# Kernel optimization log

Measured on AMD Instinct MI355X. Metric: run time of the kernel, lower is better.

Reference implementation:

```python
import jax, jax.numpy as jnp
import numpy as np

LAT_T, LAT_H, LAT_W = 16, 44, 80  # hard-coded latent grid in preprocess_mask


def _preprocess_mask(mask):
    """mask: [T, H, W, B] float video mask -> [B, S] binary mask, S = 16*44*80.
    Mirrors torch trilinear interpolate (align_corners=False) per temporal chunk."""
    m = jnp.transpose(mask, (3, 0, 1, 2))[:, None]  # [B,1,T,H,W]
    B, _, T, _, _ = m.shape
    tgt = (B, 1, 1, LAT_H, LAT_W)
    pieces = [jax.image.resize(m[:, :, :1], tgt, 'trilinear', antialias=False)]
    for wi in range(1, T, 8):
        pieces.append(jax.image.resize(m[:, :, wi:wi + 8], tgt, 'trilinear', antialias=False))
    mm = jnp.concatenate(pieces, axis=2)[:, 0]  # [B,16,44,80]
    return (mm > 0.5).astype(jnp.float32).reshape(B, -1)  # [B,S]


def setup_inputs() -> dict:
    key = jax.random.key(0)
    ks = jax.random.split(key, 6)
    B, S, H, D, P, R = 1, 56320, 8, 64, 128, 2
    T, MH, MW = 121, 88, 160
    return {
        'q': jax.random.normal(ks[0], (B, S, H, D), jnp.float32),
        'k': jax.random.normal(ks[1], (B, P, H, D), jnp.float32),
        'v': jax.random.normal(ks[2], (B, P, H, D), jnp.float32),
        'regional_k': jax.random.normal(ks[3], (R, B, P, H, D), jnp.float32),
        'regional_v': jax.random.normal(ks[4], (R, B, P, H, D), jnp.float32),
        'region_masks': jax.random.uniform(ks[5], (R, T, MH, MW, B), jnp.float32),
    }


def reference(q, k, v, regional_k, regional_v, region_masks):
    B, S, H, D = q.shape
    P = k.shape[1]
    R = regional_k.shape[0]
    scale = D ** -0.5
    base_ratio = 0.5

    # per-region binary masks over the latent sequence: [R,B,S]
    masks = jnp.stack([_preprocess_mask(region_masks[i]) for i in range(R)], axis=0)
    masks_b = masks > 0.5
    global_mask = masks.sum(axis=0) == 0  # [B,S] queries covered by no region
    # allowed[b,s,r]: segment r of combined KV (r=0 global prompt, r>=1 region r-1)
    allowed = jnp.concatenate([global_mask[..., None], jnp.moveaxis(masks_b, 0, -1)], axis=-1)  # [B,S,R+1]

    combined_k = jnp.concatenate([k[None], regional_k], axis=0)  # [R+1,B,P,H,D]
    combined_v = jnp.concatenate([v[None], regional_v], axis=0)

    # regional pass: scores [B,H,S,R+1,P], additive -inf bias per segment
    scores = jnp.einsum('bshd,rbphd->bhsrp', q, combined_k) * scale
    scores = jnp.where(allowed[:, None, :, :, None], scores, -jnp.inf)
    p = jax.nn.softmax(scores.reshape(B, H, S, (R + 1) * P), axis=-1)
    out_reg = jnp.einsum('bhsrp,rbphd->bshd', p.reshape(B, H, S, R + 1, P), combined_v)

    # base pass: plain cross attention over the global prompt
    s_base = jnp.einsum('bshd,bphd->bhsp', q, k) * scale
    out_base = jnp.einsum('bhsp,bphd->bshd', jax.nn.softmax(s_base, axis=-1), v)

    out = out_reg * (1.0 - base_ratio) + out_base * base_ratio
    return out.reshape(B, S, H * D)
```

## Files before the change

### kernel.cpp

```cpp
#include <hip/hip_runtime.h>

typedef short short8  __attribute__((ext_vector_type(8)));
typedef float f32x4   __attribute__((ext_vector_type(4)));
typedef float f32x16  __attribute__((ext_vector_type(16)));

#define MFMA32(A,B,C) __builtin_amdgcn_mfma_f32_32x32x16_bf16((A),(B),(C),0,0,0)

__device__ __forceinline__ short bf16bits(float f){
  return (short)__builtin_bit_cast(unsigned short, static_cast<__bf16>(f));
}

#define EXP_SCORE(s, BIAS) __builtin_amdgcn_exp2f(__builtin_fmaf((s), 0.18033688011112042f, (BIAS)))
#define EXP_C2 (-11.541560327111707f)

__global__ __launch_bounds__(256) void prep_kernel(const float* __restrict__ rm,
                                                   const float* __restrict__ k,
                                                   const float* __restrict__ v,
                                                   const float* __restrict__ rk,
                                                   const float* __restrict__ rv,
                                                   unsigned* __restrict__ allowed,
                                                   unsigned short* __restrict__ Kb,
                                                   unsigned short* __restrict__ VT){
  const int bid = blockIdx.x;
  if (bid < 220){
    int s = bid*256 + threadIdx.x;
    if (s >= 56320) return;
    int t = s / 3520;
    int rem = s - t*3520;
    int i = rem / 80;
    int j = rem - i*80;
    int y = 2*i, x = 2*j;
    bool bin[2];
    #pragma unroll
    for (int r=0;r<2;r++){
      const float* base = rm + (size_t)r*121*88*160;
      float acc;
      if (t == 0){
        const float* p0 = base + (size_t)(0*88 + y)*160 + x;
        acc = 0.25f*(p0[0]+p0[1]+p0[160]+p0[161]);
      } else {
        const float* pa = base + (size_t)((8*t-4)*88 + y)*160 + x;
        const float* pb = base + (size_t)((8*t-3)*88 + y)*160 + x;
        acc = 0.125f*(pa[0]+pa[1]+pa[160]+pa[161] + pb[0]+pb[1]+pb[160]+pb[161]);
      }
      bin[r] = acc > 0.5f;
    }
    unsigned bits = (bin[0]||bin[1]) ? 0u : 1u;
    if (bin[0]) bits |= 2u;
    if (bin[1]) bits |= 4u;
    allowed[s] = bits;
  } else {
    int idx = (bid-220)*256 + threadIdx.x;
    if (idx >= 3*128*8*64) return;
    int d   = idx & 63;
    int h   = (idx >> 6) & 7;
    int p   = (idx >> 9) & 127;
    int seg = idx >> 16;
    int low = idx & 65535;
    float kv_, vv_;
    if (seg == 0){ kv_ = k[low];                          vv_ = v[low]; }
    else         { kv_ = rk[(size_t)(seg-1)*65536 + low]; vv_ = rv[(size_t)(seg-1)*65536 + low]; }
    const int kk = seg*128 + p;
    {
      const int f  = d >> 4, hi = (d >> 3) & 1, j = d & 7;
      Kb[(size_t)h*24576 + ((kk>>5)*4 + f)*512
         + (hi*32 + (kk&31))*8 + j] = (unsigned short)bf16bits(kv_);
    }
    {
      const int kap = kk & 31;
      const int kh  = kap >> 4, rem = kap & 15;
      const int hi  = (rem >> 2) & 1;
      const int e   = (rem & 3) + 4*(rem >> 3);
      const int dblk = d >> 5;
      VT[(size_t)h*24576 + ((kk>>5)*4 + dblk*2 + kh)*512
         + (hi*32 + (d&31))*8 + e] = (unsigned short)bf16bits(vv_);
    }
  }
}

__global__ __launch_bounds__(256)
void attn_kernel(const float* __restrict__ q,
                 const unsigned* __restrict__ allowed,
                 const unsigned short* __restrict__ Kb,
                 const unsigned short* __restrict__ VT,
                 float* __restrict__ out){
  const int h    = blockIdx.y;
  const int wave = threadIdx.x >> 6;
  const int lane = threadIdx.x & 63;
  const int qc   = lane & 31;
  const int hi   = lane >> 5;

  __shared__ __align__(16) char Ks[49152];

  const int s = blockIdx.x*128 + wave*32 + qc;

  {
    typedef __attribute__((address_space(1))) const unsigned int gu32_t;
    typedef __attribute__((address_space(3))) unsigned int lu32_t;
    const char* kg = (const char*)Kb + (size_t)h*49152;
    #pragma unroll
    for (int i=0;i<12;i++){
      const int ub = wave*12288 + i*1024;
      __builtin_amdgcn_global_load_lds((gu32_t*)(kg + ub + lane*16),
                                       (lu32_t*)(Ks + ub), 16, 0, 0);
    }
  }

  const unsigned ab = allowed[s];
  const float* qp = q + ((size_t)s*8 + h)*64 + hi*8;
  short8 qf0, qf1, qf2, qf3;
  {
    f32x4 a, b;
    a = *(const f32x4*)(qp);      b = *(const f32x4*)(qp+4);
    #pragma unroll
    for (int j=0;j<4;j++){ qf0[j]=bf16bits(a[j]); qf0[4+j]=bf16bits(b[j]); }
    a = *(const f32x4*)(qp+16);   b = *(const f32x4*)(qp+20);
    #pragma unroll
    for (int j=0;j<4;j++){ qf1[j]=bf16bits(a[j]); qf1[4+j]=bf16bits(b[j]); }
    a = *(const f32x4*)(qp+32);   b = *(const f32x4*)(qp+36);
    #pragma unroll
    for (int j=0;j<4;j++){ qf2[j]=bf16bits(a[j]); qf2[4+j]=bf16bits(b[j]); }
    a = *(const f32x4*)(qp+48);   b = *(const f32x4*)(qp+52);
    #pragma unroll
    for (int j=0;j<4;j++){ qf3[j]=bf16bits(a[j]); qf3[4+j]=bf16bits(b[j]); }
  }

  const char* kfb = Ks + lane*16;
  const char* vgf = (const char*)VT + (size_t)h*49152 + lane*16;

  short8 v0, v1, v2, v3;
#define VLOAD(kc)                                                     \
  v0 = *(const short8*)(vgf + ((kc)*4+0)*1024);                       \
  v1 = *(const short8*)(vgf + ((kc)*4+1)*1024);                       \
  v2 = *(const short8*)(vgf + ((kc)*4+2)*1024);                       \
  v3 = *(const short8*)(vgf + ((kc)*4+3)*1024);                       \
  __builtin_amdgcn_sched_barrier(0x38F);

#define CHUNK(kc, LSUM, BIAS, A0, A1)                                 \
  {                                                                   \
    short8 kf0 = *(const short8*)(kfb + ((kc)*4+0)*1024);             \
    short8 kf1 = *(const short8*)(kfb + ((kc)*4+1)*1024);             \
    short8 kf2 = *(const short8*)(kfb + ((kc)*4+2)*1024);             \
    short8 kf3 = *(const short8*)(kfb + ((kc)*4+3)*1024);             \
    f32x16 sa = {0,0,0,0,0,0,0,0,0,0,0,0,0,0,0,0};                    \
    sa = MFMA32(kf0, qf0, sa);                                        \
    sa = MFMA32(kf1, qf1, sa);                                        \
    sa = MFMA32(kf2, qf2, sa);                                        \
    sa = MFMA32(kf3, qf3, sa);                                        \
    short8 pf0, pf1;                                                  \
    _Pragma("unroll")                                                 \
    for (int r=0;r<8;r++){                                            \
      float e0 = EXP_SCORE(sa[r],   BIAS); LSUM += e0; pf0[r] = bf16bits(e0); \
      float e1 = EXP_SCORE(sa[8+r], BIAS); LSUM += e1; pf1[r] = bf16bits(e1); \
    }                                                                 \
    A0 = MFMA32(v0, pf0, A0);                                         \
    A0 = MFMA32(v1, pf1, A0);                                         \
    A1 = MFMA32(v2, pf0, A1);                                         \
    A1 = MFMA32(v3, pf1, A1);                                         \
  }

  VLOAD(0);

  __syncthreads();

  const float bias1 = ((ab>>1)&1u) ? EXP_C2 : -3.0e38f;
  const float bias2 = ((ab>>2)&1u) ? EXP_C2 : -3.0e38f;

  float lb = 0.f, lr = 0.f;
  f32x16 aB0 = {0,0,0,0,0,0,0,0,0,0,0,0,0,0,0,0};
  f32x16 aB1 = {0,0,0,0,0,0,0,0,0,0,0,0,0,0,0,0};
  f32x16 aR0 = {0,0,0,0,0,0,0,0,0,0,0,0,0,0,0,0};
  f32x16 aR1 = {0,0,0,0,0,0,0,0,0,0,0,0,0,0,0,0};

  CHUNK(0, lb, EXP_C2, aB0, aB1); VLOAD(1);
  CHUNK(1, lb, EXP_C2, aB0, aB1); VLOAD(2);
  CHUNK(2, lb, EXP_C2, aB0, aB1); VLOAD(3);
  CHUNK(3, lb, EXP_C2, aB0, aB1); VLOAD(4);

  CHUNK(4,  lr, bias1, aR0, aR1); VLOAD(5);
  CHUNK(5,  lr, bias1, aR0, aR1); VLOAD(6);
  CHUNK(6,  lr, bias1, aR0, aR1); VLOAD(7);
  CHUNK(7,  lr, bias1, aR0, aR1); VLOAD(8);
  CHUNK(8,  lr, bias2, aR0, aR1); VLOAD(9);
  CHUNK(9,  lr, bias2, aR0, aR1); VLOAD(10);
  CHUNK(10, lr, bias2, aR0, aR1); VLOAD(11);
  CHUNK(11, lr, bias2, aR0, aR1);

  lb += __shfl_xor(lb, 32);
  lr += __shfl_xor(lr, 32);

  const float invb = 0.5f/lb;
  const float lreg = ((ab&1u)? lb : 0.f) + lr;
  const float invr = 0.5f/lreg;
  const float cA   = invb + ((ab&1u)? invr : 0.f);

  float* ob = out + (size_t)s*512 + h*64 + hi*4;
  #pragma unroll
  for (int g=0; g<4; ++g){
    f32x4 o0, o1;
    #pragma unroll
    for (int r=0;r<4;r++){
      o0[r] = aB0[g*4+r]*cA + aR0[g*4+r]*invr;
      o1[r] = aB1[g*4+r]*cA + aR1[g*4+r]*invr;
    }
    *(f32x4*)(ob + g*8)      = o0;
    *(f32x4*)(ob + 32 + g*8) = o1;
  }
}

extern "C" void kernel_launch(void* const* d_in, const int* in_sizes, int n_in,
                              void* d_out, int out_size, void* d_ws, size_t ws_size,
                              hipStream_t stream) {
  const float* q  = (const float*)d_in[0];
  const float* k  = (const float*)d_in[1];
  const float* v  = (const float*)d_in[2];
  const float* rk = (const float*)d_in[3];
  const float* rv = (const float*)d_in[4];
  const float* rm = (const float*)d_in[5];
  float* out = (float*)d_out;

  char* ws = (char*)d_ws;
  unsigned*       allowed = (unsigned*)ws;
  unsigned short* Kb      = (unsigned short*)(ws + 225280);
  unsigned short* VT      = (unsigned short*)(ws + 225280 + 393216);

  prep_kernel<<<988, 256, 0, stream>>>(rm, k, v, rk, rv, allowed, Kb, VT);
  dim3 grid(440, 8);
  attn_kernel<<<grid, 256, 0, stream>>>(q, allowed, Kb, VT, out);
}
```

Before: 257.9 us.

## Stage K and V in LDS and run a persistent grid looping over query chunks

Result: slower. 389.4 us (+51.0%).

```diff
diff --git a/kernel.cpp b/kernel.cpp
--- a/kernel.cpp
+++ b/kernel.cpp
@@ -78,63 +78,46 @@
   }
 }
 
-__global__ __launch_bounds__(256)
+__global__ __launch_bounds__(512, 2)
 void attn_kernel(const float* __restrict__ q,
                  const unsigned* __restrict__ allowed,
                  const unsigned short* __restrict__ Kb,
                  const unsigned short* __restrict__ VT,
                  float* __restrict__ out){
-  const int h    = blockIdx.y;
+  extern __shared__ __align__(16) char smem[];
+  char* Ks = smem;
+  char* Vs = smem + 49152;
+
+  const int bid  = blockIdx.x;
+  const int h    = bid & 7;
+  const int cb   = bid >> 3;
   const int wave = threadIdx.x >> 6;
   const int lane = threadIdx.x & 63;
   const int qc   = lane & 31;
   const int hi   = lane >> 5;
 
-  __shared__ __align__(16) char Ks[49152];
-
-  const int s = blockIdx.x*128 + wave*32 + qc;
-
   {
     typedef __attribute__((address_space(1))) const unsigned int gu32_t;
     typedef __attribute__((address_space(3))) unsigned int lu32_t;
-    const char* kg = (const char*)Kb + (size_t)h*49152;
+    const char* src;
+    char* dst;
+    if (wave < 4){
+      src = (const char*)Kb + (size_t)h*49152 + wave*12288;
+      dst = Ks + wave*12288;
+    } else {
+      src = (const char*)VT + (size_t)h*49152 + (wave-4)*12288;
+      dst = Vs + (wave-4)*12288;
+    }
     #pragma unroll
     for (int i=0;i<12;i++){
-      const int ub = wave*12288 + i*1024;
-      __builtin_amdgcn_global_load_lds((gu32_t*)(kg + ub + lane*16),
-                                       (lu32_t*)(Ks + ub), 16, 0, 0);
-    }
-  }
-
-  const unsigned ab = allowed[s];
-  const float* qp = q + ((size_t)s*8 + h)*64 + hi*8;
-  short8 qf0, qf1, qf2, qf3;
-  {
-    f32x4 a, b;
-    a = *(const f32x4*)(qp);      b = *(const f32x4*)(qp+4);
-    #pragma unroll
-    for (int j=0;j<4;j++){ qf0[j]=bf16bits(a[j]); qf0[4+j]=bf16bits(b[j]); }
-    a = *(const f32x4*)(qp+16);   b = *(const f32x4*)(qp+20);
-    #pragma unroll
-    for (int j=0;j<4;j++){ qf1[j]=bf16bits(a[j]); qf1[4+j]=bf16bits(b[j]); }
-    a = *(const f32x4*)(qp+32);   b = *(const f32x4*)(qp+36);
-    #pragma unroll
-    for (int j=0;j<4;j++){ qf2[j]=bf16bits(a[j]); qf2[4+j]=bf16bits(b[j]); }
-    a = *(const f32x4*)(qp+48);   b = *(const f32x4*)(qp+52);
-    #pragma unroll
-    for (int j=0;j<4;j++){ qf3[j]=bf16bits(a[j]); qf3[4+j]=bf16bits(b[j]); }
-  }
+      __builtin_amdgcn_global_load_lds((gu32_t*)(src + i*1024 + lane*16),
+                                       (lu32_t*)(dst + i*1024), 16, 0, 0);
+    }
+  }
+  __syncthreads();
 
   const char* kfb = Ks + lane*16;
-  const char* vgf = (const char*)VT + (size_t)h*49152 + lane*16;
-
-  short8 v0, v1, v2, v3;
-#define VLOAD(kc)                                                     \
-  v0 = *(const short8*)(vgf + ((kc)*4+0)*1024);                       \
-  v1 = *(const short8*)(vgf + ((kc)*4+1)*1024);                       \
-  v2 = *(const short8*)(vgf + ((kc)*4+2)*1024);                       \
-  v3 = *(const short8*)(vgf + ((kc)*4+3)*1024);                       \
-  __builtin_amdgcn_sched_barrier(0x38F);
+  const char* vfb = Vs + lane*16;
 
 #define CHUNK(kc, LSUM, BIAS, A0, A1)                                 \
   {                                                                   \
@@ -142,6 +125,10 @@
     short8 kf1 = *(const short8*)(kfb + ((kc)*4+1)*1024);             \
     short8 kf2 = *(const short8*)(kfb + ((kc)*4+2)*1024);             \
     short8 kf3 = *(const short8*)(kfb + ((kc)*4+3)*1024);             \
+    short8 v0  = *(const short8*)(vfb + ((kc)*4+0)*1024);             \
+    short8 v1  = *(const short8*)(vfb + ((kc)*4+1)*1024);             \
+    short8 v2  = *(const short8*)(vfb + ((kc)*4+2)*1024);             \
+    short8 v3  = *(const short8*)(vfb + ((kc)*4+3)*1024);             \
     f32x16 sa = {0,0,0,0,0,0,0,0,0,0,0,0,0,0,0,0};                    \
     sa = MFMA32(kf0, qf0, sa);                                        \
     sa = MFMA32(kf1, qf1, sa);                                        \
@@ -159,52 +146,67 @@
     A1 = MFMA32(v3, pf1, A1);                                         \
   }
 
-  VLOAD(0);
-
-  __syncthreads();
-
-  const float bias1 = ((ab>>1)&1u) ? EXP_C2 : -3.0e38f;
-  const float bias2 = ((ab>>2)&1u) ? EXP_C2 : -3.0e38f;
-
-  float lb = 0.f, lr = 0.f;
-  f32x16 aB0 = {0,0,0,0,0,0,0,0,0,0,0,0,0,0,0,0};
-  f32x16 aB1 = {0,0,0,0,0,0,0,0,0,0,0,0,0,0,0,0};
-  f32x16 aR0 = {0,0,0,0,0,0,0,0,0,0,0,0,0,0,0,0};
-  f32x16 aR1 = {0,0,0,0,0,0,0,0,0,0,0,0,0,0,0,0};
-
-  CHUNK(0, lb, EXP_C2, aB0, aB1); VLOAD(1);
-  CHUNK(1, lb, EXP_C2, aB0, aB1); VLOAD(2);
-  CHUNK(2, lb, EXP_C2, aB0, aB1); VLOAD(3);
-  CHUNK(3, lb, EXP_C2, aB0, aB1); VLOAD(4);
-
-  CHUNK(4,  lr, bias1, aR0, aR1); VLOAD(5);
-  CHUNK(5,  lr, bias1, aR0, aR1); VLOAD(6);
-  CHUNK(6,  lr, bias1, aR0, aR1); VLOAD(7);
-  CHUNK(7,  lr, bias1, aR0, aR1); VLOAD(8);
-  CHUNK(8,  lr, bias2, aR0, aR1); VLOAD(9);
-  CHUNK(9,  lr, bias2, aR0, aR1); VLOAD(10);
-  CHUNK(10, lr, bias2, aR0, aR1); VLOAD(11);
-  CHUNK(11, lr, bias2, aR0, aR1);
-
-  lb += __shfl_xor(lb, 32);
-  lr += __shfl_xor(lr, 32);
-
-  const float invb = 0.5f/lb;
-  const float lreg = ((ab&1u)? lb : 0.f) + lr;
-  const float invr = 0.5f/lreg;
-  const float cA   = invb + ((ab&1u)? invr : 0.f);
-
-  float* ob = out + (size_t)s*512 + h*64 + hi*4;
-  #pragma unroll
-  for (int g=0; g<4; ++g){
-    f32x4 o0, o1;
-    #pragma unroll
-    for (int r=0;r<4;r++){
-      o0[r] = aB0[g*4+r]*cA + aR0[g*4+r]*invr;
-      o1[r] = aB1[g*4+r]*cA + aR1[g*4+r]*invr;
-    }
-    *(f32x4*)(ob + g*8)      = o0;
-    *(f32x4*)(ob + 32 + g*8) = o1;
+  #pragma unroll 1
+  for (int c = cb; c < 220; c += 32){
+    const int s = c*256 + wave*32 + qc;
+
+    const unsigned ab = allowed[s];
+    const float* qp = q + ((size_t)s*8 + h)*64 + hi*8;
+    f32x4 qa0 = *(const f32x4*)(qp);      f32x4 qb0 = *(const f32x4*)(qp+4);
+    f32x4 qa1 = *(const f32x4*)(qp+16);   f32x4 qb1 = *(const f32x4*)(qp+20);
+    f32x4 qa2 = *(const f32x4*)(qp+32);   f32x4 qb2 = *(const f32x4*)(qp+36);
+    f32x4 qa3 = *(const f32x4*)(qp+48);   f32x4 qb3 = *(const f32x4*)(qp+52);
+    short8 qf0, qf1, qf2, qf3;
+    #pragma unroll
+    for (int j=0;j<4;j++){
+      qf0[j]=bf16bits(qa0[j]); qf0[4+j]=bf16bits(qb0[j]);
+      qf1[j]=bf16bits(qa1[j]); qf1[4+j]=bf16bits(qb1[j]);
+      qf2[j]=bf16bits(qa2[j]); qf2[4+j]=bf16bits(qb2[j]);
+      qf3[j]=bf16bits(qa3[j]); qf3[4+j]=bf16bits(qb3[j]);
+    }
+
+    const float bias1 = ((ab>>1)&1u) ? EXP_C2 : -3.0e38f;
+    const float bias2 = ((ab>>2)&1u) ? EXP_C2 : -3.0e38f;
+
+    float lb = 0.f, lr = 0.f;
+    f32x16 aB0 = {0,0,0,0,0,0,0,0,0,0,0,0,0,0,0,0};
+    f32x16 aB1 = {0,0,0,0,0,0,0,0,0,0,0,0,0,0,0,0};
+    f32x16 aR0 = {0,0,0,0,0,0,0,0,0,0,0,0,0,0,0,0};
+    f32x16 aR1 = {0,0,0,0,0,0,0,0,0,0,0,0,0,0,0,0};
+
+    CHUNK(0,  lb, EXP_C2, aB0, aB1);
+    CHUNK(1,  lb, EXP_C2, aB0, aB1);
+    CHUNK(2,  lb, EXP_C2, aB0, aB1);
+    CHUNK(3,  lb, EXP_C2, aB0, aB1);
+    CHUNK(4,  lr, bias1,  aR0, aR1);
+    CHUNK(5,  lr, bias1,  aR0, aR1);
+    CHUNK(6,  lr, bias1,  aR0, aR1);
+    CHUNK(7,  lr, bias1,  aR0, aR1);
+    CHUNK(8,  lr, bias2,  aR0, aR1);
+    CHUNK(9,  lr, bias2,  aR0, aR1);
+    CHUNK(10, lr, bias2,  aR0, aR1);
+    CHUNK(11, lr, bias2,  aR0, aR1);
+
+    lb += __shfl_xor(lb, 32);
+    lr += __shfl_xor(lr, 32);
+
+    const float invb = 0.5f/lb;
+    const float lreg = ((ab&1u)? lb : 0.f) + lr;
+    const float invr = 0.5f/lreg;
+    const float cA   = invb + ((ab&1u)? invr : 0.f);
+
+    float* ob = out + (size_t)s*512 + h*64 + hi*4;
+    #pragma unroll
+    for (int g=0; g<4; ++g){
+      f32x4 o0, o1;
+      #pragma unroll
+      for (int r=0;r<4;r++){
+        o0[r] = aB0[g*4+r]*cA + aR0[g*4+r]*invr;
+        o1[r] = aB1[g*4+r]*cA + aR1[g*4+r]*invr;
+      }
+      *(f32x4*)(ob + g*8)      = o0;
+      *(f32x4*)(ob + 32 + g*8) = o1;
+    }
   }
 }
 
@@ -224,7 +226,13 @@
   unsigned short* Kb      = (unsigned short*)(ws + 225280);
   unsigned short* VT      = (unsigned short*)(ws + 225280 + 393216);
 
+  static bool attr_done = false;
+  if (!attr_done){
+    hipFuncSetAttribute(reinterpret_cast<const void*>(attn_kernel),
+                        hipFuncAttributeMaxDynamicSharedMemorySize, 98304);
+    attr_done = true;
+  }
+
   prep_kernel<<<988, 256, 0, stream>>>(rm, k, v, rk, rv, allowed, Kb, VT);
-  dim3 grid(440, 8);
-  attn_kernel<<<grid, 256, 0, stream>>>(q, allowed, Kb, VT, out);
-}
+  attn_kernel<<<256, 512, 98304, stream>>>(q, allowed, Kb, VT, out);
+}
```
